# Performance work log

Hardware: AMD Instinct MI355X
Metric: run time of the kernel (lower is better)

Reference implementation:

```python
import jax, jax.numpy as jnp
import numpy as np

N_BINS = 11

def _normalize(x):
    # F.normalize(p=2, eps=1e-10) over the last (feature) axis
    n = jnp.linalg.norm(x, axis=-1, keepdims=True)
    return x / jnp.maximum(n, 1e-10)

def _ngram_conv(x, W, b):
    # x: (B,L,D), W: (n,D,C), b: (C,) -> (B,L-n+1,C); Conv2d(1,C,(n,D)) + ReLU, then +1e-9
    n, L = W.shape[0], x.shape[1]
    xs = jnp.stack([x[:, i:L - n + 1 + i, :] for i in range(n)], axis=2)  # (B,L',n,D)
    return jax.nn.relu(jnp.einsum('blnd,ndc->blc', xs, W) + b) + 1e-9

def _attn_conv(a, w, b):
    # a: (B,L,1), w: (n,), b: (1,) -> (B,L-n+1,1); Conv2d(1,1,(n,1)) + ReLU
    n, L = w.shape[0], a.shape[1]
    s = sum(w[i] * a[:, i:L - n + 1 + i, 0] for i in range(n))
    return jax.nn.relu(s + b)[:, :, None]

def _intersect(q, d, aq, ad, mu, sigma):
    # q: (B,Lq,C), d: (B,Ld,C), aq: (B,Lq,1), ad: (B,Ld,1), mu/sigma: (1,1,1,NB)
    sim = jnp.einsum('bqc,bdc->bqd', q, d)[..., None]          # (B,Lq,Ld,1)
    k = jnp.exp(-(sim - mu) ** 2 / (sigma ** 2) / 2.0)         # (B,Lq,Ld,NB)
    ps = jnp.sum(k * ad[:, None, :, :], axis=2)                # (B,Lq,NB)
    lps = jnp.log(jnp.maximum(ps, 1e-10)) * 0.01 * aq
    return jnp.sum(lps, axis=1)                                # (B,NB)

def _forward(wrd_emb, attn_table, W_uni, b_uni, W_bi, b_bi, W_tri, b_tri,
             wa_uni, ba_uni, wa_bi, ba_bi, wa_tri, ba_tri, W_dense, b_dense,
             mu, sigma, inputs_qwt, inputs_dwt, inputs_qwm, inputs_dwm):
    qw = wrd_emb[inputs_qwt]                                   # (B,Lq,D)
    dw = wrd_emb[inputs_dwt]                                   # (B,Ld,D)
    attn = attn_table[inputs_qwt]                              # (B,Lq,1) frozen IDF
    q_u = _normalize(_ngram_conv(qw, W_uni, b_uni))
    q_b = _normalize(_ngram_conv(qw, W_bi, b_bi))
    q_t = _normalize(_ngram_conv(qw, W_tri, b_tri))
    d_u = _normalize(_ngram_conv(dw, W_uni, b_uni))
    d_b = _normalize(_ngram_conv(dw, W_bi, b_bi))
    d_t = _normalize(_ngram_conv(dw, W_tri, b_tri))
    Lq, Ld = inputs_qwt.shape[1], inputs_dwt.shape[1]
    mq = inputs_qwm[:, :, None]
    aq_u = mq[:, :Lq] * _attn_conv(attn, wa_uni, ba_uni)
    aq_b = mq[:, :Lq - 1] * _attn_conv(attn, wa_bi, ba_bi)
    aq_t = mq[:, :Lq - 2] * _attn_conv(attn, wa_tri, ba_tri)
    md = inputs_dwm[:, :, None]
    ad_u, ad_b, ad_t = md[:, :Ld], md[:, :Ld - 1], md[:, :Ld - 2]
    pools = [
        _intersect(q_u, d_u, aq_u, ad_u, mu, sigma),
        _intersect(q_u, d_t, aq_u, ad_t, mu, sigma),
        _intersect(q_u, d_b, aq_u, ad_b, mu, sigma),
        _intersect(q_b, d_u, aq_b, ad_u, mu, sigma),
        _intersect(q_t, d_u, aq_t, ad_u, mu, sigma),
        _intersect(q_b, d_b, aq_b, ad_b, mu, sigma),
        _intersect(q_b, d_t, aq_b, ad_t, mu, sigma),
        _intersect(q_t, d_b, aq_t, ad_b, mu, sigma),
        _intersect(q_t, d_t, aq_t, ad_t, mu, sigma),
    ]
    lp = jnp.concatenate(pools, axis=1)                        # (B, 9*N_BINS)
    return jnp.tanh(lp @ W_dense + b_dense)[:, 0]              # (B,)


def setup_inputs() -> dict:
    key = jax.random.key(0)
    ks = jax.random.split(key, 12)
    B, Lq, Ld, D, V, C = 128, 32, 512, 300, 50000, 128
    mu = jnp.array([1.0, 0.9, 0.7, 0.5, 0.3, 0.1, -0.1, -0.3, -0.5, -0.7, -0.9], jnp.float32).reshape(1, 1, 1, N_BINS)
    sigma = jnp.array([0.001] + [0.1] * 10, jnp.float32).reshape(1, 1, 1, N_BINS)
    return {
        'wrd_emb': jax.random.normal(ks[0], (V, D), jnp.float32) * 0.1,
        'attn_table': jax.random.uniform(ks[1], (V, 1), jnp.float32),
        'W_uni': jax.random.normal(ks[2], (1, D, C), jnp.float32) * 0.05,
        'b_uni': jnp.zeros((C,), jnp.float32),
        'W_bi': jax.random.normal(ks[3], (2, D, C), jnp.float32) * 0.05,
        'b_bi': jnp.zeros((C,), jnp.float32),
        'W_tri': jax.random.normal(ks[4], (3, D, C), jnp.float32) * 0.05,
        'b_tri': jnp.zeros((C,), jnp.float32),
        'wa_uni': jax.random.uniform(ks[5], (1,), jnp.float32, 0.1, 1.0),
        'ba_uni': jnp.zeros((1,), jnp.float32),
        'wa_bi': jax.random.uniform(ks[6], (2,), jnp.float32, 0.1, 1.0),
        'ba_bi': jnp.zeros((1,), jnp.float32),
        'wa_tri': jax.random.uniform(ks[7], (3,), jnp.float32, 0.1, 1.0),
        'ba_tri': jnp.zeros((1,), jnp.float32),
        'W_dense': jax.random.normal(ks[8], (9 * N_BINS, 1), jnp.float32) * 0.1,
        'b_dense': jnp.zeros((1,), jnp.float32),
        'mu': mu, 'sigma': sigma,
        'inputs_qwt': jax.random.randint(ks[9], (B, Lq), 0, V),
        'inputs_dwt': jax.random.randint(ks[10], (B, Ld), 0, V),
        'inputs_qwm': jnp.ones((B, Lq), jnp.float32),
        'inputs_dwm': jnp.ones((B, Ld), jnp.float32),
    }


def reference(wrd_emb, attn_table, W_uni, b_uni, W_bi, b_bi, W_tri, b_tri, wa_uni, ba_uni, wa_bi, ba_bi, wa_tri, ba_tri, W_dense, b_dense, mu, sigma, inputs_qwt, inputs_dwt, inputs_qwm, inputs_dwm):
    return _forward(wrd_emb, attn_table, W_uni, b_uni, W_bi, b_bi, W_tri, b_tri, wa_uni, ba_uni, wa_bi, ba_bi, wa_tri, ba_tri, W_dense, b_dense, mu, sigma, inputs_qwt, inputs_dwt, inputs_qwm, inputs_dwm)
```

## Files before the change

kernel.cpp:

```cpp
#include <hip/hip_runtime.h>
#include <hip/hip_bf16.h>

typedef __bf16 bf16_t;
typedef __bf16 bf16x8 __attribute__((ext_vector_type(8)));
typedef float f32x16 __attribute__((ext_vector_type(16)));

#define NV 50000

#define OFF_EMB 0UL
#define SZ_EMB  (50001UL*320*2)
#define OFF_WT  (OFF_EMB + SZ_EMB)
#define SZ_WT   (128UL*1920*2)
#define OFF_QN  (OFF_WT + SZ_WT)
#define SZ_QN   (128UL*3*32*128*2)
#define OFF_DN  (OFF_QN + SZ_QN)
#define SZ_DN   (128UL*3*512*128*2)
#define OFF_AQ  (OFF_DN + SZ_DN)
#define SZ_AQ   (128UL*3*32*4)
#define OFF_LP  (OFF_AQ + SZ_AQ)

#if __has_builtin(__builtin_amdgcn_global_load_lds)
__device__ __forceinline__ void gll16(const void* g, void* l) {
  __builtin_amdgcn_global_load_lds((const __attribute__((address_space(1))) unsigned int*)g,
                                   (__attribute__((address_space(3))) unsigned int*)l, 16, 0, 0);
}
#else
__device__ __forceinline__ void gll16(const void* g, void* l) {
  *(uint4*)l = *(const uint4*)g;
}
#endif

__global__ __launch_bounds__(256) void k_prep_emb(const float* __restrict__ emb,
                                                  bf16_t* __restrict__ out) {
  long t = (long)blockIdx.x * 256 + threadIdx.x;
  if (t >= 50001L * 40) return;
  int r = (int)(t / 40), c0 = (int)(t % 40) * 8;
  bf16x8 v;
#pragma unroll
  for (int j = 0; j < 8; j++) {
    int c = c0 + j;
    float f = (r < 50000 && c < 300) ? emb[(long)r * 300 + c] : 0.f;
    v[j] = (bf16_t)f;
  }
  *(bf16x8*)(out + (long)r * 320 + c0) = v;
}

__global__ __launch_bounds__(256) void k_prep_wt(const float* __restrict__ Wu,
                                                 const float* __restrict__ Wb,
                                                 const float* __restrict__ Wt,
                                                 bf16_t* __restrict__ wt) {
  int t = blockIdx.x * 256 + threadIdx.x;
  if (t >= 30720) return;
  int g, local;
  if (t < 5120)       { g = 0; local = t; }
  else if (t < 15360) { g = 1; local = t - 5120; }
  else                { g = 2; local = t - 15360; }
  int kp = 320 * (g + 1);
  int c = local / (kp >> 3), k0 = (local % (kp >> 3)) * 8;
  const float* W = (g == 0) ? Wu : (g == 1) ? Wb : Wt;
  long base = (g == 0) ? 0L : (g == 1) ? 128L * 320 : 128L * 960;
  bf16x8 v;
#pragma unroll
  for (int j = 0; j < 8; j++) {
    int k = k0 + j, n = k / 320, ks = k % 320;
    float f = (ks < 300) ? W[((long)n * 300 + ks) * 128 + c] : 0.f;
    v[j] = (bf16_t)f;
  }
  *(bf16x8*)(wt + base + (long)c * kp + k0) = v;
}

__global__ __launch_bounds__(64) void k_prep_aq(const float* __restrict__ attn_tab,
                                                const int* __restrict__ qwt,
                                                const float* __restrict__ qwm,
                                                const float* wa_u, const float* ba_u,
                                                const float* wa_b, const float* ba_b,
                                                const float* wa_t, const float* ba_t,
                                                float* __restrict__ aq) {
  int b = blockIdx.x, q = threadIdx.x;
  int qc = q < 32 ? q : 31;
  float a0 = attn_tab[qwt[b * 32 + qc]];
  float a1 = __shfl_down(a0, 1);
  float a2 = __shfl_down(a0, 2);
  if (q < 32) {
    float mq = qwm[b * 32 + q];
    float u  = mq * fmaxf(wa_u[0] * a0 + ba_u[0], 0.f);
    float bb = (q < 31) ? mq * fmaxf(wa_b[0] * a0 + wa_b[1] * a1 + ba_b[0], 0.f) : 0.f;
    float tt = (q < 30) ? mq * fmaxf(wa_t[0] * a0 + wa_t[1] * a1 + wa_t[2] * a2 + ba_t[0], 0.f) : 0.f;
    aq[(b * 3 + 0) * 32 + q] = u;
    aq[(b * 3 + 1) * 32 + q] = bb;
    aq[(b * 3 + 2) * 32 + q] = tt;
  }
}

__global__ __launch_bounds__(256, 3) void k_conv(const bf16_t* __restrict__ embb,
                                                 const bf16_t* __restrict__ wtg,
                                                 const int* __restrict__ qwt,
                                                 const int* __restrict__ dwt,
                                                 const float* __restrict__ b_uni,
                                                 const float* __restrict__ b_bi,
                                                 const float* __restrict__ b_tri,
                                                 bf16_t* __restrict__ qn,
                                                 bf16_t* __restrict__ dn) {
  __shared__ int tok[136];
  __shared__ __align__(16) char embc[12288];
  __shared__ __align__(16) char wc[24576];
  const int tid = threadIdx.x;
  const int w = tid >> 6, lane = tid & 63, lr = lane & 31, l5 = lane >> 5;
  const int blk = blockIdx.x;
  const bool isq = (blk >= 512);
  int b = 0, p0 = 0, b0 = 0, rowbase;
  if (!isq) { b = blk >> 2; p0 = (blk & 3) << 7; rowbase = w * 32; }
  else      { b0 = (blk - 512) << 2; rowbase = w * 34; }

  if (tid < 136) {
    int t;
    if (!isq) { int p = p0 + tid; t = (p < 512) ? dwt[b * 512 + p] : NV; }
    else      { int bb = tid / 34, pos = tid - bb * 34; t = (pos < 32) ? qwt[(b0 + bb) * 32 + pos] : NV; }
    tok[tid] = t;
  }
  __syncthreads();

  const bf16_t* srcE[3]; char* dstE[3];
#pragma unroll
  for (int t = 0; t < 3; t++) {
    int i = tid + t * 256;
    int r = i >> 2; if (r > 135) r = 135;
    int slot = i & 3;
    srcE[t] = embb + (long)tok[r] * 320 + ((slot ^ ((r >> 1) & 3)) << 3);
    dstE[t] = embc + i * 16;
  }

#pragma unroll
  for (int g = 0; g < 3; g++) {
    const int kp = 320 * (g + 1);
    const long wbase = (g == 0) ? 0L : (g == 1) ? 128L * 320 : 128L * 960;
    const int nw = 2 * (g + 1);
    const bf16_t* srcW[6]; char* dstW[6];
#pragma unroll
    for (int j = 0; j < 6; j++) {
      if (j < nw) {
        int i2 = tid + j * 256;
        int n = i2 >> 9, c = (i2 >> 2) & 127, slot = i2 & 3;
        srcW[j] = wtg + wbase + (long)c * kp + n * 320 + ((slot ^ ((c >> 1) & 3)) << 3);
        dstW[j] = wc + i2 * 16;
      }
    }

    f32x16 acc[4];
#pragma unroll
    for (int nt = 0; nt < 4; nt++)
#pragma unroll
      for (int r2 = 0; r2 < 16; r2++) acc[nt][r2] = 0.f;

    for (int kk = 0; kk < 10; kk++) {
#pragma unroll
      for (int t = 0; t < 3; t++) gll16(srcE[t] + kk * 32, dstE[t]);
#pragma unroll
      for (int j = 0; j < 6; j++)
        if (j < nw) gll16(srcW[j] + kk * 32, dstW[j]);
      __syncthreads();

#pragma unroll
      for (int n = 0; n <= g; n++) {
        int arow = rowbase + lr + n;
        int aswz = ((arow >> 1) & 3) << 4;
        const char* ab = embc + arow * 64;
        bf16x8 a0 = *(const bf16x8*)(ab + ((l5 << 4) ^ aswz));
        bf16x8 a1 = *(const bf16x8*)(ab + ((32 + (l5 << 4)) ^ aswz));
#pragma unroll
        for (int nt = 0; nt < 4; nt++) {
          int crow = nt * 32 + lr;
          int bswz = ((crow >> 1) & 3) << 4;
          const char* bb2 = wc + n * 8192 + crow * 64;
          bf16x8 w0 = *(const bf16x8*)(bb2 + ((l5 << 4) ^ bswz));
          bf16x8 w1 = *(const bf16x8*)(bb2 + ((32 + (l5 << 4)) ^ bswz));
          acc[nt] = __builtin_amdgcn_mfma_f32_32x32x16_bf16(a0, w0, acc[nt], 0, 0, 0);
          acc[nt] = __builtin_amdgcn_mfma_f32_32x32x16_bf16(a1, w1, acc[nt], 0, 0, 0);
        }
      }
      __syncthreads();
    }

    const float* bp = (g == 0) ? b_uni : (g == 1) ? b_bi : b_tri;
    float bias[4];
#pragma unroll
    for (int nt = 0; nt < 4; nt++) bias[nt] = bp[nt * 32 + lr];
#pragma unroll
    for (int nt = 0; nt < 4; nt++)
#pragma unroll
      for (int r2 = 0; r2 < 16; r2++) {
        float v = acc[nt][r2] + bias[nt];
        acc[nt][r2] = fmaxf(v, 0.f) + 1e-9f;
      }
    float scale[16];
#pragma unroll
    for (int r2 = 0; r2 < 16; r2++) {
      float s = acc[0][r2] * acc[0][r2] + acc[1][r2] * acc[1][r2] +
                acc[2][r2] * acc[2][r2] + acc[3][r2] * acc[3][r2];
      s += __shfl_xor(s, 1);  s += __shfl_xor(s, 2);  s += __shfl_xor(s, 4);
      s += __shfl_xor(s, 8);  s += __shfl_xor(s, 16);
      scale[r2] = 1.f / fmaxf(sqrtf(s), 1e-10f);
    }
    const int L = isq ? 32 : 512;
    const int lim = L - g;
#pragma unroll
    for (int r2 = 0; r2 < 16; r2++) {
      int R = (r2 & 3) + ((r2 >> 2) << 3) + (l5 << 2);
      int pos, bi_;
      if (!isq) { pos = p0 + w * 32 + R; bi_ = b; }
      else      { pos = R; bi_ = b0 + w; }
      bool valid = pos < lim;
      bf16_t* o = (isq ? qn : dn) + (((long)bi_ * 3 + g) * L + pos) * 128 + lr;
#pragma unroll
      for (int nt = 0; nt < 4; nt++) {
        float vv = valid ? acc[nt][r2] * scale[r2] : 0.f;
        o[nt * 32] = (bf16_t)vv;
      }
    }
  }
}

__global__ __launch_bounds__(256, 4) void k_intersect(const bf16_t* __restrict__ qn,
                                                      const bf16_t* __restrict__ dn,
                                                      const float* __restrict__ aq,
                                                      const float* __restrict__ dwm,
                                                      const float* __restrict__ mu,
                                                      const float* __restrict__ sigma,
                                                      float* __restrict__ lp) {
  __shared__ __align__(16) char qs[8192];
  __shared__ float dwm_s[512];
  __shared__ float ps_red[4][32][11];
  __shared__ float lps_s[32][11];
  const int tid = threadIdx.x;
  const int w = tid >> 6, lane = tid & 63, lr = lane & 31, l5 = lane >> 5;
  const int b = blockIdx.x, pool = blockIdx.y;
  const int gq = (0x29640 >> (2 * pool)) & 3;
  const int gd = (0x26418 >> (2 * pool)) & 3;

  const bf16_t* qbase = qn + ((long)b * 3 + gq) * 32 * 128;
  for (int i = tid; i < 512; i += 256) {
    int q = i >> 4, j = i & 15;
    bf16x8 v = *(const bf16x8*)(qbase + q * 128 + j * 8);
    *(bf16x8*)(qs + q * 256 + ((j ^ (q & 15)) << 4)) = v;
  }
  for (int i = tid; i < 512; i += 256) dwm_s[i] = dwm[b * 512 + i];

  float c2[11], A_[11], B_[11];
#pragma unroll
  for (int i2 = 0; i2 < 11; i2++) {
    float m = mu[i2], s = sigma[i2];
    float c = -0.72134752f / (s * s);
    c2[i2] = c;  A_[i2] = -2.f * c * m;  B_[i2] = c * m * m;
  }
  float ps[11];
#pragma unroll
  for (int i2 = 0; i2 < 11; i2++) ps[i2] = 0.f;
  __syncthreads();

  const int lim_d = 512 - gd;
  const bf16_t* dgbase = dn + ((long)b * 3 + gd) * 512 * 128;
  for (int it = 0; it < 4; it++) {
    int d0 = it * 128 + w * 32;
    f32x16 acc;
#pragma unroll
    for (int i2 = 0; i2 < 16; i2++) acc[i2] = 0.f;
    const bf16_t* dptr = dgbase + (long)(d0 + lr) * 128;
#pragma unroll
    for (int kk = 0; kk < 4; kk++) {
      bf16x8 a0 = *(const bf16x8*)(dptr + kk * 32 + l5 * 8);
      bf16x8 a1 = *(const bf16x8*)(dptr + kk * 32 + 16 + l5 * 8);
      int koff0 = kk * 64 + (l5 << 4);
      bf16x8 b0 = *(const bf16x8*)(qs + lr * 256 + (koff0 ^ ((lr & 15) << 4)));
      bf16x8 b1 = *(const bf16x8*)(qs + lr * 256 + ((koff0 + 32) ^ ((lr & 15) << 4)));
      acc = __builtin_amdgcn_mfma_f32_32x32x16_bf16(a0, b0, acc, 0, 0, 0);
      acc = __builtin_amdgcn_mfma_f32_32x32x16_bf16(a1, b1, acc, 0, 0, 0);
    }
#pragma unroll
    for (int r2 = 0; r2 < 16; r2++) {
      int dr = d0 + (r2 & 3) + ((r2 >> 2) << 3) + (l5 << 2);
      float ad = (dr < lim_d) ? dwm_s[dr] : 0.f;
      float s = acc[r2];
      float s2 = s * s;
#pragma unroll
      for (int bin = 0; bin < 11; bin++) {
        float t = fmaf(s2, c2[bin], fmaf(s, A_[bin], B_[bin]));
        ps[bin] = fmaf(exp2f(t), ad, ps[bin]);
      }
    }
  }
#pragma unroll
  for (int bin = 0; bin < 11; bin++) ps[bin] += __shfl_xor(ps[bin], 32);
  if (l5 == 0) {
#pragma unroll
    for (int bin = 0; bin < 11; bin++) ps_red[w][lr][bin] = ps[bin];
  }
  __syncthreads();
  const float* aqb = aq + ((long)b * 3 + gq) * 32;
  for (int t = tid; t < 352; t += 256) {
    int q = t / 11, bin = t - q * 11;
    float p = ps_red[0][q][bin] + ps_red[1][q][bin] + ps_red[2][q][bin] + ps_red[3][q][bin];
    lps_s[q][bin] = logf(fmaxf(p, 1e-10f)) * 0.01f * aqb[q];
  }
  __syncthreads();
  if (tid < 11) {
    float s = 0.f;
    for (int q = 0; q < 32; q++) s += lps_s[q][tid];
    lp[(long)b * 99 + pool * 11 + tid] = s;
  }
}

__global__ __launch_bounds__(128) void k_final(const float* __restrict__ lp,
                                               const float* __restrict__ Wd,
                                               const float* __restrict__ bd,
                                               float* __restrict__ out) {
  int b = threadIdx.x;
  float s = bd[0];
  for (int j = 0; j < 99; j++) s = fmaf(lp[b * 99 + j], Wd[j], s);
  out[b] = tanhf(s);
}

extern "C" void kernel_launch(void* const* d_in, const int* in_sizes, int n_in,
                              void* d_out, int out_size, void* d_ws, size_t ws_size,
                              hipStream_t stream) {
  const float* emb   = (const float*)d_in[0];
  const float* attn  = (const float*)d_in[1];
  const float* Wu    = (const float*)d_in[2];
  const float* bu    = (const float*)d_in[3];
  const float* Wb    = (const float*)d_in[4];
  const float* bb    = (const float*)d_in[5];
  const float* Wt    = (const float*)d_in[6];
  const float* bt    = (const float*)d_in[7];
  const float* wau   = (const float*)d_in[8];
  const float* bau   = (const float*)d_in[9];
  const float* wab   = (const float*)d_in[10];
  const float* bab   = (const float*)d_in[11];
  const float* wat   = (const float*)d_in[12];
  const float* bat   = (const float*)d_in[13];
  const float* Wd    = (const float*)d_in[14];
  const float* bd    = (const float*)d_in[15];
  const float* mu    = (const float*)d_in[16];
  const float* sigma = (const float*)d_in[17];
  const int*   qwt   = (const int*)d_in[18];
  const int*   dwt   = (const int*)d_in[19];
  const float* qwm   = (const float*)d_in[20];
  const float* dwm   = (const float*)d_in[21];

  char* ws = (char*)d_ws;
  bf16_t* embb = (bf16_t*)(ws + OFF_EMB);
  bf16_t* wtg  = (bf16_t*)(ws + OFF_WT);
  bf16_t* qn   = (bf16_t*)(ws + OFF_QN);
  bf16_t* dn   = (bf16_t*)(ws + OFF_DN);
  float*  aq   = (float*)(ws + OFF_AQ);
  float*  lp   = (float*)(ws + OFF_LP);
  float*  out  = (float*)d_out;

  hipLaunchKernelGGL(k_prep_emb, dim3(7813), dim3(256), 0, stream, emb, embb);
  hipLaunchKernelGGL(k_prep_wt,  dim3(120),  dim3(256), 0, stream, Wu, Wb, Wt, wtg);
  hipLaunchKernelGGL(k_prep_aq,  dim3(128),  dim3(64),  0, stream,
                     attn, qwt, qwm, wau, bau, wab, bab, wat, bat, aq);
  hipLaunchKernelGGL(k_conv, dim3(544), dim3(256), 0, stream,
                     embb, wtg, qwt, dwt, bu, bb, bt, qn, dn);
  hipLaunchKernelGGL(k_intersect, dim3(128, 9), dim3(256), 0, stream,
                     qn, dn, aq, dwm, mu, sigma, lp);
  hipLaunchKernelGGL(k_final, dim3(1), dim3(128), 0, stream, lp, Wd, bd, out);
}
```

Baseline: 316.3 us.

## Fuse uni/bi/tri n-gram convolutions into one K loop sharing embedding tiles

Merges the three sequential per-n-gram GEMM passes into a single K loop. Each embedding tile is loaded once and reused across all three filter widths, with all six weight slices staged together in a larger LDS buffer. This removes the embedding reloads and two of the three sets of loop barriers. In exchange it keeps three accumulator sets live (192 floats per lane) and doubles weight LDS, so launch bounds drop to 2 blocks per SM, which reduces occupancy and adds spill risk.

Result: slower. 323.5 us (+2.3%).

```diff
diff --git a/kernel.cpp b/kernel.cpp
--- a/kernel.cpp
+++ b/kernel.cpp
@@ -92,7 +92,7 @@
   }
 }
 
-__global__ __launch_bounds__(256, 3) void k_conv(const bf16_t* __restrict__ embb,
+__global__ __launch_bounds__(256, 2) void k_conv(const bf16_t* __restrict__ embb,
                                                  const bf16_t* __restrict__ wtg,
                                                  const int* __restrict__ qwt,
                                                  const int* __restrict__ dwt,
@@ -103,7 +103,7 @@
                                                  bf16_t* __restrict__ dn) {
   __shared__ int tok[136];
   __shared__ __align__(16) char embc[12288];
-  __shared__ __align__(16) char wc[24576];
+  __shared__ __align__(16) char wc[49152];
   const int tid = threadIdx.x;
   const int w = tid >> 6, lane = tid & 63, lr = lane & 31, l5 = lane >> 5;
   const int blk = blockIdx.x;
@@ -130,57 +130,65 @@
     dstE[t] = embc + i * 16;
   }
 
-#pragma unroll
-  for (int g = 0; g < 3; g++) {
-    const int kp = 320 * (g + 1);
-    const long wbase = (g == 0) ? 0L : (g == 1) ? 128L * 320 : 128L * 960;
-    const int nw = 2 * (g + 1);
-    const bf16_t* srcW[6]; char* dstW[6];
-#pragma unroll
-    for (int j = 0; j < 6; j++) {
-      if (j < nw) {
-        int i2 = tid + j * 256;
-        int n = i2 >> 9, c = (i2 >> 2) & 127, slot = i2 & 3;
-        srcW[j] = wtg + wbase + (long)c * kp + n * 320 + ((slot ^ ((c >> 1) & 3)) << 3);
-        dstW[j] = wc + i2 * 16;
-      }
-    }
-
-    f32x16 acc[4];
+  const bf16_t* srcW[12]; char* dstW[12];
+  {
+    const int g6[6] = {0, 1, 1, 2, 2, 2};
+    const int n6[6] = {0, 0, 1, 0, 1, 2};
+#pragma unroll
+    for (int j = 0; j < 12; j++) {
+      int i2 = tid + j * 256;
+      int pair = j >> 1;
+      int g = g6[pair], n = n6[pair];
+      int kp = 320 * (g + 1);
+      long wbase = (g == 0) ? 0L : (g == 1) ? 128L * 320 : 128L * 960;
+      int c = (i2 >> 2) & 127, slot = i2 & 3;
+      srcW[j] = wtg + wbase + (long)c * kp + n * 320 + ((slot ^ ((c >> 1) & 3)) << 3);
+      dstW[j] = wc + i2 * 16;
+    }
+  }
+
+  f32x16 acc[3][4];
+#pragma unroll
+  for (int g = 0; g < 3; g++)
 #pragma unroll
     for (int nt = 0; nt < 4; nt++)
 #pragma unroll
-      for (int r2 = 0; r2 < 16; r2++) acc[nt][r2] = 0.f;
-
-    for (int kk = 0; kk < 10; kk++) {
-#pragma unroll
-      for (int t = 0; t < 3; t++) gll16(srcE[t] + kk * 32, dstE[t]);
-#pragma unroll
-      for (int j = 0; j < 6; j++)
-        if (j < nw) gll16(srcW[j] + kk * 32, dstW[j]);
-      __syncthreads();
-
-#pragma unroll
-      for (int n = 0; n <= g; n++) {
-        int arow = rowbase + lr + n;
-        int aswz = ((arow >> 1) & 3) << 4;
-        const char* ab = embc + arow * 64;
-        bf16x8 a0 = *(const bf16x8*)(ab + ((l5 << 4) ^ aswz));
-        bf16x8 a1 = *(const bf16x8*)(ab + ((32 + (l5 << 4)) ^ aswz));
+      for (int r2 = 0; r2 < 16; r2++) acc[g][nt][r2] = 0.f;
+
+  for (int kk = 0; kk < 10; kk++) {
+#pragma unroll
+    for (int t = 0; t < 3; t++) gll16(srcE[t] + kk * 32, dstE[t]);
+#pragma unroll
+    for (int j = 0; j < 12; j++) gll16(srcW[j] + kk * 32, dstW[j]);
+    __syncthreads();
+
+#pragma unroll
+    for (int n = 0; n < 3; n++) {
+      int arow = rowbase + lr + n;
+      int aswz = ((arow >> 1) & 3) << 4;
+      const char* ab = embc + arow * 64;
+      bf16x8 a0 = *(const bf16x8*)(ab + ((l5 << 4) ^ aswz));
+      bf16x8 a1 = *(const bf16x8*)(ab + ((32 + (l5 << 4)) ^ aswz));
+#pragma unroll
+      for (int g = n; g < 3; g++) {
+        const int pair = (g == 0) ? 0 : (g == 1) ? 1 + n : 3 + n;
 #pragma unroll
         for (int nt = 0; nt < 4; nt++) {
           int crow = nt * 32 + lr;
           int bswz = ((crow >> 1) & 3) << 4;
-          const char* bb2 = wc + n * 8192 + crow * 64;
+          const char* bb2 = wc + pair * 8192 + crow * 64;
           bf16x8 w0 = *(const bf16x8*)(bb2 + ((l5 << 4) ^ bswz));
           bf16x8 w1 = *(const bf16x8*)(bb2 + ((32 + (l5 << 4)) ^ bswz));
-          acc[nt] = __builtin_amdgcn_mfma_f32_32x32x16_bf16(a0, w0, acc[nt], 0, 0, 0);
-          acc[nt] = __builtin_amdgcn_mfma_f32_32x32x16_bf16(a1, w1, acc[nt], 0, 0, 0);
+          acc[g][nt] = __builtin_amdgcn_mfma_f32_32x32x16_bf16(a0, w0, acc[g][nt], 0, 0, 0);
+          acc[g][nt] = __builtin_amdgcn_mfma_f32_32x32x16_bf16(a1, w1, acc[g][nt], 0, 0, 0);
         }
       }
-      __syncthreads();
-    }
-
+    }
+    __syncthreads();
+  }
+
+#pragma unroll
+  for (int g = 0; g < 3; g++) {
     const float* bp = (g == 0) ? b_uni : (g == 1) ? b_bi : b_tri;
     float bias[4];
 #pragma unroll
@@ -189,14 +197,14 @@
     for (int nt = 0; nt < 4; nt++)
 #pragma unroll
       for (int r2 = 0; r2 < 16; r2++) {
-        float v = acc[nt][r2] + bias[nt];
-        acc[nt][r2] = fmaxf(v, 0.f) + 1e-9f;
+        float v = acc[g][nt][r2] + bias[nt];
+        acc[g][nt][r2] = fmaxf(v, 0.f) + 1e-9f;
       }
     float scale[16];
 #pragma unroll
     for (int r2 = 0; r2 < 16; r2++) {
-      float s = acc[0][r2] * acc[0][r2] + acc[1][r2] * acc[1][r2] +
-                acc[2][r2] * acc[2][r2] + acc[3][r2] * acc[3][r2];
+      float s = acc[g][0][r2] * acc[g][0][r2] + acc[g][1][r2] * acc[g][1][r2] +
+                acc[g][2][r2] * acc[g][2][r2] + acc[g][3][r2] * acc[g][3][r2];
       s += __shfl_xor(s, 1);  s += __shfl_xor(s, 2);  s += __shfl_xor(s, 4);
       s += __shfl_xor(s, 8);  s += __shfl_xor(s, 16);
       scale[r2] = 1.f / fmaxf(sqrtf(s), 1e-10f);
@@ -213,7 +221,7 @@
       bf16_t* o = (isq ? qn : dn) + (((long)bi_ * 3 + g) * L + pos) * 128 + lr;
 #pragma unroll
       for (int nt = 0; nt < 4; nt++) {
-        float vv = valid ? acc[nt][r2] * scale[r2] : 0.f;
+        float vv = valid ? acc[g][nt][r2] * scale[r2] : 0.f;
         o[nt * 32] = (bf16_t)vv;
       }
     }
```
